# Kernel tuning notes

Measured on AMD Instinct MI355X. Metric: run time of the kernel, lower is better.

Reference implementation:

```python
import jax, jax.numpy as jnp
import numpy as np

GROUPS = 32
EPS = 1e-5


def group_norm(x, gamma, beta):
    B, C, D, H, W = x.shape
    xr = x.reshape(B, GROUPS, C // GROUPS, D, H, W)
    mean = xr.mean(axis=(2, 3, 4, 5), keepdims=True)
    var = xr.var(axis=(2, 3, 4, 5), keepdims=True)
    xn = (xr - mean) * jax.lax.rsqrt(var + EPS)
    xn = xn.reshape(B, C, D, H, W)
    return xn * gamma[None, :, None, None, None] + beta[None, :, None, None, None]


def conv1x1(h, w, b):
    # 1x1x1 Conv3d == channel matmul. w: [O, C], b: [O]
    return jnp.einsum('oc,bcdhw->bodhw', w, h) + b[None, :, None, None, None]


def setup_inputs() -> dict:
    key = jax.random.key(0)
    ks = jax.random.split(key, 10)
    B, C, D, H, W = 2, 128, 16, 16, 16
    x = jax.random.normal(ks[0], (B, C, D, H, W), dtype=jnp.float32)
    gn_w = jnp.ones((C,), dtype=jnp.float32)
    gn_b = jnp.zeros((C,), dtype=jnp.float32)
    # xavier_uniform for [C, C, 1, 1, 1] conv: fan_in = fan_out = C
    lim = float(np.sqrt(6.0 / (C + C)))
    wq = jax.random.uniform(ks[1], (C, C), jnp.float32, -lim, lim)
    wk = jax.random.uniform(ks[2], (C, C), jnp.float32, -lim, lim)
    wv = jax.random.uniform(ks[3], (C, C), jnp.float32, -lim, lim)
    wp = jax.random.uniform(ks[4], (C, C), jnp.float32, -lim, lim) * 1e-05
    bq = jnp.zeros((C,), jnp.float32)
    bk = jnp.zeros((C,), jnp.float32)
    bv = jnp.zeros((C,), jnp.float32)
    bp = jnp.zeros((C,), jnp.float32)
    return {"x": x, "gn_w": gn_w, "gn_b": gn_b, "wq": wq, "bq": bq,
            "wk": wk, "bk": bk, "wv": wv, "bv": bv, "wp": wp, "bp": bp}


def reference(x, gn_w, gn_b, wq, bq, wk, bk, wv, bv, wp, bp):
    B, C, D, H, W = x.shape
    N = D * H * W
    h = group_norm(x, gn_w, gn_b)
    q = conv1x1(h, wq, bq)
    k = conv1x1(h, wk, bk)
    v = conv1x1(h, wv, bv)
    q = q.transpose(0, 2, 3, 4, 1).reshape(B, N, C)   # [B, N, C]
    k = k.reshape(B, C, N)                            # [B, C, N]
    v = v.transpose(0, 2, 3, 4, 1).reshape(B, N, C)   # [B, N, C]
    w = jnp.einsum('bnc,bcm->bnm', q, k) * (C ** -0.5)  # [B, N, N]
    w = jax.nn.softmax(w, axis=-1)
    h = jnp.einsum('bnm,bmc->bnc', w, v)              # [B, N, C]
    h = h.reshape(B, D, H, W, C).transpose(0, 4, 1, 2, 3)
    h = conv1x1(h, wp, bp)
    return x + h
```

## Files before the change

kernel.cpp:

```cpp
#include <hip/hip_runtime.h>
#include <math.h>

#define CC 128
#define NN 4096
#define BB 2
#define NGROUPS 32
#define CPG 4
#define GSIZE (CPG*NN)
#define KSPLIT 2

typedef __attribute__((ext_vector_type(8))) __bf16 bf16x8;
typedef __attribute__((ext_vector_type(4))) float floatx4;

__device__ __forceinline__ unsigned short f2bf(float f) {
  union { float f; unsigned u; } v; v.f = f;
  unsigned r = v.u + 0x7fff + ((v.u >> 16) & 1);
  return (unsigned short)(r >> 16);
}
__device__ __forceinline__ float bf2f(unsigned short u) {
  return __uint_as_float(((unsigned)u) << 16);
}


__global__ void gn_stats_kernel(const float* __restrict__ x, float2* __restrict__ stats) {
  int bid = blockIdx.x;
  int t = threadIdx.x;
  const float4* base = (const float4*)(x + (size_t)bid * 4096);
  float4 v = base[t];
  float s  = v.x + v.y + v.z + v.w;
  float ss = v.x*v.x + v.y*v.y + v.z*v.z + v.w*v.w;
  #pragma unroll
  for (int off = 1; off < 64; off <<= 1) {
    s  += __shfl_xor(s, off);
    ss += __shfl_xor(ss, off);
  }
  __shared__ float sred[4], ssred[4];
  if ((t & 63) == 0) { sred[t >> 6] = s; ssred[t >> 6] = ss; }
  __syncthreads();
  if (t == 0)
    stats[bid] = make_float2(sred[0]+sred[1]+sred[2]+sred[3],
                             ssred[0]+ssred[1]+ssred[2]+ssred[3]);
}

__global__ void prep_kernel(const float2* __restrict__ stats,
                            const float* __restrict__ gamma, const float* __restrict__ beta,
                            const float* __restrict__ wq, const float* __restrict__ bq,
                            const float* __restrict__ wk, const float* __restrict__ wv,
                            const float* __restrict__ wp,
                            float* __restrict__ ab_a, float* __restrict__ ab_b,
                            float* __restrict__ bqs,
                            unsigned short* __restrict__ wqb, unsigned short* __restrict__ wkb,
                            unsigned short* __restrict__ wvb, unsigned short* __restrict__ wpb) {
  const float sc = 0.08838834764831845f;
  int t = threadIdx.x;
  if (blockIdx.x == 64) {
    if (t < BB*NGROUPS) {
      float su = 0.f, ssq = 0.f;
      #pragma unroll
      for (int j = 0; j < 4; j++) { float2 p = stats[t*4 + j]; su += p.x; ssq += p.y; }
      float mean = su * (1.0f/GSIZE);
      float var  = ssq * (1.0f/GSIZE) - mean*mean;
      float rstd = rsqrtf(var + 1e-5f);
      int b = t / NGROUPS, g = t % NGROUPS;
      #pragma unroll
      for (int j = 0; j < 4; j++) {
        int c = g*4 + j;
        float a = rstd * gamma[c];
        ab_a[b*CC + c] = a;
        ab_b[b*CC + c] = beta[c] - mean * a;
      }
    }
    if (t < CC) bqs[t] = bq[t] * sc;
  } else {
    int i = blockIdx.x * 256 + t;
    int id = i >> 12, local = i & 4095;
    const float* src = id==0 ? wq : id==1 ? wk : id==2 ? wv : wp;
    unsigned short* dst = id==0 ? wqb : id==1 ? wkb : id==2 ? wvb : wpb;
    float s = (id == 0) ? sc : 1.0f;
    float4 v = ((const float4*)src)[local];
    unsigned p0 = (unsigned)f2bf(v.x*s) | ((unsigned)f2bf(v.y*s) << 16);
    unsigned p1 = (unsigned)f2bf(v.z*s) | ((unsigned)f2bf(v.w*s) << 16);
    ((uint2*)dst)[local] = make_uint2(p0, p1);
  }
}

__global__ __launch_bounds__(256, 2) void qkv_kernel(
    const float* __restrict__ x,
    const float* __restrict__ ab_a, const float* __restrict__ ab_b,
    const unsigned short* __restrict__ wqb, const unsigned short* __restrict__ wkb,
    const unsigned short* __restrict__ wvb,
    const float* __restrict__ bqs, const float* __restrict__ bk, const float* __restrict__ bv,
    unsigned short* __restrict__ q, unsigned short* __restrict__ k, unsigned short* __restrict__ v) {
  int z = blockIdx.z, b = blockIdx.y, n0 = blockIdx.x * 32;
  const unsigned short* wsel = z==0 ? wqb : z==1 ? wkb : wvb;
  const float* bias          = z==0 ? bqs : z==1 ? bk  : bv;
  unsigned short* outp       = z==0 ? q   : z==1 ? k   : v;
  __shared__ unsigned short hs[32][130];
  __shared__ unsigned short vs[32][136];
  int t = threadIdx.x;
  #pragma unroll
  for (int j = 0; j < 16; j++) {
    int idx = j*256 + t;
    int c = idx >> 5, n = idx & 31;
    float xv = x[((size_t)b*CC + c)*NN + n0 + n];
    hs[n][c] = f2bf(ab_a[b*CC + c]*xv + ab_b[b*CC + c]);
  }
  __syncthreads();
  int w = t >> 6, lane = t & 63, quad = lane >> 4, c = lane & 15;
  int o0 = w * 32;
  floatx4 acc[2][2];
  #pragma unroll
  for (int rt = 0; rt < 2; rt++)
    #pragma unroll
    for (int ct = 0; ct < 2; ct++) acc[rt][ct] = (floatx4){0.f,0.f,0.f,0.f};
  #pragma unroll
  for (int ks = 0; ks < 4; ks++) {
    bf16x8 af[2];
    af[0] = *(const bf16x8*)&hs[c     ][ks*32 + quad*8];
    af[1] = *(const bf16x8*)&hs[16 + c][ks*32 + quad*8];
    #pragma unroll
    for (int ct = 0; ct < 2; ct++) {
      bf16x8 bfr = *(const bf16x8*)(wsel + (size_t)(o0 + ct*16 + c)*CC + ks*32 + quad*8);
      acc[0][ct] = __builtin_amdgcn_mfma_f32_16x16x32_bf16(af[0], bfr, acc[0][ct], 0, 0, 0);
      acc[1][ct] = __builtin_amdgcn_mfma_f32_16x16x32_bf16(af[1], bfr, acc[1][ct], 0, 0, 0);
    }
  }
  if (z < 2) {
    size_t base = (size_t)b*NN*CC + ((size_t)(n0 >> 4))*2048 + w*512;
    #pragma unroll
    for (int ct = 0; ct < 2; ct++) {
      float bi = bias[o0 + ct*16 + c];
      #pragma unroll
      for (int rt = 0; rt < 2; rt++)
        #pragma unroll
        for (int r = 0; r < 4; r++)
          outp[base + rt*2048 + (quad*4 + r)*32 + ct*16 + c] = f2bf(acc[rt][ct][r] + bi);
    }
  } else {
    #pragma unroll
    for (int ct = 0; ct < 2; ct++) {
      float bi = bias[o0 + ct*16 + c];
      #pragma unroll
      for (int rt = 0; rt < 2; rt++)
        #pragma unroll
        for (int r = 0; r < 4; r++)
          vs[rt*16 + quad*4 + r][o0 + ct*16 + c] = f2bf(acc[rt][ct][r] + bi);
    }
    __syncthreads();
    int ct = t >> 5;
    int rem = t & 31;
    int c16 = rem >> 1;
    int m0 = (rem & 1) * 16;
    int ch = ct*16 + c16;
    unsigned pk[8];
    #pragma unroll
    for (int j2 = 0; j2 < 8; j2++) {
      unsigned lo = vs[m0 + j2*2    ][ch];
      unsigned hi = vs[m0 + j2*2 + 1][ch];
      pk[j2] = lo | (hi << 16);
    }
    uint4* dst = (uint4*)(outp + (size_t)b*NN*CC + ((size_t)(n0 >> 5))*4096 + ct*512 + c16*32 + m0);
    dst[0] = make_uint4(pk[0], pk[1], pk[2], pk[3]);
    dst[1] = make_uint4(pk[4], pk[5], pk[6], pk[7]);
  }
}

__global__ __launch_bounds__(256, 2) void attn_kernel(
    const unsigned short* __restrict__ qm,
    const unsigned short* __restrict__ km,
    const unsigned short* __restrict__ vm,
    unsigned short* __restrict__ Opart,
    float* __restrict__ lpart) {
  int b    = blockIdx.z;
  int kh   = blockIdx.y;
  int row0 = blockIdx.x * 32;
  int t    = threadIdx.x;
  int w    = t >> 6, lane = t & 63, quad = lane >> 4, c = lane & 15;

  __shared__ unsigned short shmem[4][32][132];
  __shared__ float lred[4][32];
  unsigned short (*Pl)[72] = (unsigned short (*)[72])&shmem[w][0][0];

  int fragoff = c*32 + quad*8;

  bf16x8 qa[2][4];
  const unsigned short* qbase = qm + (size_t)b*NN*CC + ((size_t)(row0 >> 4))*2048;
  #pragma unroll
  for (int rt = 0; rt < 2; rt++)
    #pragma unroll
    for (int ks = 0; ks < 4; ks++)
      qa[rt][ks] = *(const bf16x8*)(qbase + rt*2048 + ks*512 + fragoff);

  floatx4 O[2][8];
  #pragma unroll
  for (int rt = 0; rt < 2; rt++)
    #pragma unroll
    for (int ct = 0; ct < 8; ct++) O[rt][ct] = (floatx4){0.f,0.f,0.f,0.f};
  float lsum[2][4];
  #pragma unroll
  for (int rt = 0; rt < 2; rt++)
    #pragma unroll
    for (int r = 0; r < 4; r++) lsum[rt][r] = 0.f;

  const unsigned short* kb0 = km + (size_t)b*NN*CC;
  const unsigned short* vb0 = vm + (size_t)b*NN*CC;

  for (int it = 0; it < NN/KSPLIT/256; it++) {
    int mbase = kh*(NN/KSPLIT) + it*256 + w*64;
    const unsigned short* kt = kb0 + ((size_t)(mbase >> 4))*2048;
    const unsigned short* vt = vb0 + ((size_t)(mbase >> 5))*4096;
    floatx4 S[2][4];
    #pragma unroll
    for (int rt = 0; rt < 2; rt++)
      #pragma unroll
      for (int ct = 0; ct < 4; ct++) S[rt][ct] = (floatx4){0.f,0.f,0.f,0.f};
    #pragma unroll
    for (int ks = 0; ks < 4; ks++) {
      #pragma unroll
      for (int ct = 0; ct < 4; ct++) {
        bf16x8 kf = *(const bf16x8*)(kt + ct*2048 + ks*512 + fragoff);
        S[0][ct] = __builtin_amdgcn_mfma_f32_16x16x32_bf16(qa[0][ks], kf, S[0][ct], 0, 0, 0);
        S[1][ct] = __builtin_amdgcn_mfma_f32_16x16x32_bf16(qa[1][ks], kf, S[1][ct], 0, 0, 0);
      }
    }
    #pragma unroll
    for (int rt = 0; rt < 2; rt++) {
      #pragma unroll
      for (int ct = 0; ct < 4; ct++) {
        float e0 = __expf(S[rt][ct][0]);
        float e1 = __expf(S[rt][ct][1]);
        float e2 = __expf(S[rt][ct][2]);
        float e3 = __expf(S[rt][ct][3]);
        lsum[rt][0] += e0; lsum[rt][1] += e1;
        lsum[rt][2] += e2; lsum[rt][3] += e3;
        bool odd = (c & 1);
        float s01 = odd ? e0 : e1;
        float g01 = __shfl_xor(s01, 1);
        unsigned lo0 = __float_as_uint(odd ? g01 : e0);
        unsigned hi0 = __float_as_uint(odd ? e1 : g01);
        unsigned p0 = (hi0 & 0xffff0000u) | (lo0 >> 16);
        float s23 = odd ? e2 : e3;
        float g23 = __shfl_xor(s23, 1);
        unsigned lo1 = __float_as_uint(odd ? g23 : e2);
        unsigned hi1 = __float_as_uint(odd ? e3 : g23);
        unsigned p1 = (hi1 & 0xffff0000u) | (lo1 >> 16);
        int colpair = ct*16 + (c & ~1);
        int rowA = rt*16 + quad*4 + (odd ? 1 : 0);
        int rowB = rt*16 + quad*4 + (odd ? 3 : 2);
        *(unsigned*)&Pl[rowA][colpair] = p0;
        *(unsigned*)&Pl[rowB][colpair] = p1;
      }
    }
    #pragma unroll
    for (int ks2 = 0; ks2 < 2; ks2++) {
      bf16x8 pa0 = *(const bf16x8*)(&Pl[c     ][ks2*32 + quad*8]);
      bf16x8 pa1 = *(const bf16x8*)(&Pl[16 + c][ks2*32 + quad*8]);
      #pragma unroll
      for (int ct = 0; ct < 8; ct++) {
        bf16x8 vf = *(const bf16x8*)(vt + ks2*4096 + ct*512 + fragoff);
        O[0][ct] = __builtin_amdgcn_mfma_f32_16x16x32_bf16(pa0, vf, O[0][ct], 0, 0, 0);
        O[1][ct] = __builtin_amdgcn_mfma_f32_16x16x32_bf16(pa1, vf, O[1][ct], 0, 0, 0);
      }
    }
  }

  #pragma unroll
  for (int rt = 0; rt < 2; rt++)
    #pragma unroll
    for (int r = 0; r < 4; r++) {
      float vsum = lsum[rt][r];
      vsum += __shfl_xor(vsum, 1);
      vsum += __shfl_xor(vsum, 2);
      vsum += __shfl_xor(vsum, 4);
      vsum += __shfl_xor(vsum, 8);
      if (c == 0) lred[w][rt*16 + quad*4 + r] = vsum;
    }
  __syncthreads();
  #pragma unroll
  for (int rt = 0; rt < 2; rt++)
    #pragma unroll
    for (int ct = 0; ct < 8; ct++)
      #pragma unroll
      for (int r = 0; r < 4; r++)
        shmem[w][rt*16 + quad*4 + r][ct*16 + c] = f2bf(O[rt][ct][r]);
  __syncthreads();
  size_t pbase = (size_t)(kh*BB + b)*NN + row0;
  if (t < 32)
    lpart[pbase + t] = lred[0][t] + lred[1][t] + lred[2][t] + lred[3][t];
  int rr = t >> 3, c0 = (t & 7) * 16;
  unsigned pk[8];
  #pragma unroll
  for (int j2 = 0; j2 < 8; j2++) {
    int cc0 = c0 + j2*2;
    float v0 = bf2f(shmem[0][rr][cc0])   + bf2f(shmem[1][rr][cc0])
             + bf2f(shmem[2][rr][cc0])   + bf2f(shmem[3][rr][cc0]);
    float v1 = bf2f(shmem[0][rr][cc0+1]) + bf2f(shmem[1][rr][cc0+1])
             + bf2f(shmem[2][rr][cc0+1]) + bf2f(shmem[3][rr][cc0+1]);
    pk[j2] = (unsigned)f2bf(v0) | ((unsigned)f2bf(v1) << 16);
  }
  uint4* od = (uint4*)(Opart + (pbase + rr)*CC + c0);
  od[0] = make_uint4(pk[0], pk[1], pk[2], pk[3]);
  od[1] = make_uint4(pk[4], pk[5], pk[6], pk[7]);
}

__global__ __launch_bounds__(256, 2) void combine_kernel(
    const unsigned short* __restrict__ Opart, const float* __restrict__ lpart,
    const unsigned short* __restrict__ wpb, const float* __restrict__ bp,
    const float* __restrict__ x, float* __restrict__ out) {
  int b = blockIdx.y, n0 = blockIdx.x * 32;
  int t = threadIdx.x;
  __shared__ unsigned short hs[32][130];
  __shared__ float ps[32][132];
  __shared__ float linv[32];
  if (t < 32) {
    float l = 0.f;
    #pragma unroll
    for (int kh = 0; kh < KSPLIT; kh++)
      l += lpart[((size_t)(kh*BB + b))*NN + n0 + t];
    linv[t] = 1.f / l;
  }
  __syncthreads();
  #pragma unroll
  for (int j = 0; j < 16; j++) {
    int idx = j*256 + t;
    int n = idx >> 7, c2 = idx & 127;
    float o = 0.f;
    #pragma unroll
    for (int kh = 0; kh < KSPLIT; kh++)
      o += bf2f(Opart[((size_t)(kh*BB + b)*NN + n0 + n)*CC + c2]);
    hs[n][c2] = f2bf(o * linv[n]);
  }
  __syncthreads();
  int w = t >> 6, lane = t & 63, quad = lane >> 4, c = lane & 15;
  int o0 = w * 32;
  floatx4 acc[2][2];
  #pragma unroll
  for (int rt = 0; rt < 2; rt++)
    #pragma unroll
    for (int ct = 0; ct < 2; ct++) acc[rt][ct] = (floatx4){0.f,0.f,0.f,0.f};
  #pragma unroll
  for (int ks = 0; ks < 4; ks++) {
    bf16x8 af[2];
    af[0] = *(const bf16x8*)&hs[c     ][ks*32 + quad*8];
    af[1] = *(const bf16x8*)&hs[16 + c][ks*32 + quad*8];
    #pragma unroll
    for (int ct = 0; ct < 2; ct++) {
      bf16x8 bfr = *(const bf16x8*)(wpb + (size_t)(o0 + ct*16 + c)*CC + ks*32 + quad*8);
      acc[0][ct] = __builtin_amdgcn_mfma_f32_16x16x32_bf16(af[0], bfr, acc[0][ct], 0, 0, 0);
      acc[1][ct] = __builtin_amdgcn_mfma_f32_16x16x32_bf16(af[1], bfr, acc[1][ct], 0, 0, 0);
    }
  }
  #pragma unroll
  for (int rt = 0; rt < 2; rt++)
    #pragma unroll
    for (int ct = 0; ct < 2; ct++)
      #pragma unroll
      for (int r = 0; r < 4; r++)
        ps[rt*16 + quad*4 + r][o0 + ct*16 + c] = acc[rt][ct][r];
  __syncthreads();
  int o = t >> 1, nh = (t & 1) * 16;
  float bi = bp[o];
  const float* xr = x + ((size_t)b*CC + o)*NN + n0 + nh;
  float* orow = out + ((size_t)b*CC + o)*NN + n0 + nh;
  #pragma unroll
  for (int j4 = 0; j4 < 4; j4++) {
    float4 xv = ((const float4*)xr)[j4];
    float4 ov;
    ov.x = xv.x + ps[nh + j4*4 + 0][o] + bi;
    ov.y = xv.y + ps[nh + j4*4 + 1][o] + bi;
    ov.z = xv.z + ps[nh + j4*4 + 2][o] + bi;
    ov.w = xv.w + ps[nh + j4*4 + 3][o] + bi;
    ((float4*)orow)[j4] = ov;
  }
}

extern "C" void kernel_launch(void* const* d_in, const int* in_sizes, int n_in,
                              void* d_out, int out_size, void* d_ws, size_t ws_size,
                              hipStream_t stream) {
  const float* x    = (const float*)d_in[0];
  const float* gn_w = (const float*)d_in[1];
  const float* gn_b = (const float*)d_in[2];
  const float* wq   = (const float*)d_in[3];
  const float* bq   = (const float*)d_in[4];
  const float* wk   = (const float*)d_in[5];
  const float* bk   = (const float*)d_in[6];
  const float* wv   = (const float*)d_in[7];
  const float* bv   = (const float*)d_in[8];
  const float* wp   = (const float*)d_in[9];
  const float* bp   = (const float*)d_in[10];
  float* out = (float*)d_out;

  char* ws = (char*)d_ws;
  float2*         stats = (float2*)(ws);
  float*          ab_a  = (float*)(ws + 2048);
  float*          ab_b  = (float*)(ws + 3072);
  float*          bqs   = (float*)(ws + 4096);
  unsigned short* wqb   = (unsigned short*)(ws + 8192);
  unsigned short* wkb   = (unsigned short*)(ws + 8192 + 32768);
  unsigned short* wvb   = (unsigned short*)(ws + 8192 + 65536);
  unsigned short* wpb   = (unsigned short*)(ws + 8192 + 98304);
  unsigned short* qb    = (unsigned short*)(ws + 262144);
  unsigned short* kb    = (unsigned short*)(ws + 262144 + 2097152);
  unsigned short* vb    = (unsigned short*)(ws + 262144 + 2*2097152);
  unsigned short* Opart = (unsigned short*)(ws + 262144 + 3*2097152);
  float*          lpart = (float*)(ws + 262144 + 3*2097152 + 4194304);

  gn_stats_kernel<<<dim3(256), 256, 0, stream>>>(x, stats);
  prep_kernel    <<<dim3(65), 256, 0, stream>>>(stats, gn_w, gn_b, wq, bq, wk, wv, wp,
                                                ab_a, ab_b, bqs, wqb, wkb, wvb, wpb);
  qkv_kernel     <<<dim3(NN/32, BB, 3), 256, 0, stream>>>(x, ab_a, ab_b, wqb, wkb, wvb,
                                                          bqs, bk, bv, qb, kb, vb);
  attn_kernel    <<<dim3(NN/32, KSPLIT, BB), 256, 0, stream>>>(qb, kb, vb, Opart, lpart);
  combine_kernel <<<dim3(NN/32, BB), 256, 0, stream>>>(Opart, lpart, wpb, bp, x, out);
}
```

Measured before the change: 134.6 us.

## Merge prep into stats kernel, fold GN finalize into qkv, prefetch K fragments

The weight bf16 conversion now runs in extra blocks of the stats kernel, and the group-norm mean/rstd finalisation moves into each qkv block, computed in shared memory. This removes one kernel launch and the small prep dependency stage, at the cost of redundant per-block stats work. In the attention loop, the K fragments for the next iteration are loaded into registers while softmax and PV run, to hide global load latency. This adds register pressure from the 16-entry kfn array.

```diff
diff --git a/kernel.cpp b/kernel.cpp
--- a/kernel.cpp
+++ b/kernel.cpp
@@ -22,57 +22,32 @@
 }
 
 
-__global__ void gn_stats_kernel(const float* __restrict__ x, float2* __restrict__ stats) {
-  int bid = blockIdx.x;
+__global__ void gn_stats_kernel(const float* __restrict__ x, float2* __restrict__ stats,
+                                const float* __restrict__ wq, const float* __restrict__ wk,
+                                const float* __restrict__ wv, const float* __restrict__ wp,
+                                unsigned short* __restrict__ wqb, unsigned short* __restrict__ wkb,
+                                unsigned short* __restrict__ wvb, unsigned short* __restrict__ wpb) {
   int t = threadIdx.x;
-  const float4* base = (const float4*)(x + (size_t)bid * 4096);
-  float4 v = base[t];
-  float s  = v.x + v.y + v.z + v.w;
-  float ss = v.x*v.x + v.y*v.y + v.z*v.z + v.w*v.w;
-  #pragma unroll
-  for (int off = 1; off < 64; off <<= 1) {
-    s  += __shfl_xor(s, off);
-    ss += __shfl_xor(ss, off);
-  }
-  __shared__ float sred[4], ssred[4];
-  if ((t & 63) == 0) { sred[t >> 6] = s; ssred[t >> 6] = ss; }
-  __syncthreads();
-  if (t == 0)
-    stats[bid] = make_float2(sred[0]+sred[1]+sred[2]+sred[3],
-                             ssred[0]+ssred[1]+ssred[2]+ssred[3]);
-}
-
-__global__ void prep_kernel(const float2* __restrict__ stats,
-                            const float* __restrict__ gamma, const float* __restrict__ beta,
-                            const float* __restrict__ wq, const float* __restrict__ bq,
-                            const float* __restrict__ wk, const float* __restrict__ wv,
-                            const float* __restrict__ wp,
-                            float* __restrict__ ab_a, float* __restrict__ ab_b,
-                            float* __restrict__ bqs,
-                            unsigned short* __restrict__ wqb, unsigned short* __restrict__ wkb,
-                            unsigned short* __restrict__ wvb, unsigned short* __restrict__ wpb) {
-  const float sc = 0.08838834764831845f;
-  int t = threadIdx.x;
-  if (blockIdx.x == 64) {
-    if (t < BB*NGROUPS) {
-      float su = 0.f, ssq = 0.f;
-      #pragma unroll
-      for (int j = 0; j < 4; j++) { float2 p = stats[t*4 + j]; su += p.x; ssq += p.y; }
-      float mean = su * (1.0f/GSIZE);
-      float var  = ssq * (1.0f/GSIZE) - mean*mean;
-      float rstd = rsqrtf(var + 1e-5f);
-      int b = t / NGROUPS, g = t % NGROUPS;
-      #pragma unroll
-      for (int j = 0; j < 4; j++) {
-        int c = g*4 + j;
-        float a = rstd * gamma[c];
-        ab_a[b*CC + c] = a;
-        ab_b[b*CC + c] = beta[c] - mean * a;
-      }
-    }
-    if (t < CC) bqs[t] = bq[t] * sc;
+  if (blockIdx.x < 256) {
+    int bid = blockIdx.x;
+    const float4* base = (const float4*)(x + (size_t)bid * 4096);
+    float4 v = base[t];
+    float s  = v.x + v.y + v.z + v.w;
+    float ss = v.x*v.x + v.y*v.y + v.z*v.z + v.w*v.w;
+    #pragma unroll
+    for (int off = 1; off < 64; off <<= 1) {
+      s  += __shfl_xor(s, off);
+      ss += __shfl_xor(ss, off);
+    }
+    __shared__ float sred[4], ssred[4];
+    if ((t & 63) == 0) { sred[t >> 6] = s; ssred[t >> 6] = ss; }
+    __syncthreads();
+    if (t == 0)
+      stats[bid] = make_float2(sred[0]+sred[1]+sred[2]+sred[3],
+                               ssred[0]+ssred[1]+ssred[2]+ssred[3]);
   } else {
-    int i = blockIdx.x * 256 + t;
+    const float sc = 0.08838834764831845f;
+    int i = (blockIdx.x - 256) * 256 + t;
     int id = i >> 12, local = i & 4095;
     const float* src = id==0 ? wq : id==1 ? wk : id==2 ? wv : wp;
     unsigned short* dst = id==0 ? wqb : id==1 ? wkb : id==2 ? wvb : wpb;
@@ -85,25 +60,47 @@
 }
 
 __global__ __launch_bounds__(256, 2) void qkv_kernel(
-    const float* __restrict__ x,
-    const float* __restrict__ ab_a, const float* __restrict__ ab_b,
+    const float* __restrict__ x, const float2* __restrict__ stats,
+    const float* __restrict__ gamma, const float* __restrict__ beta,
     const unsigned short* __restrict__ wqb, const unsigned short* __restrict__ wkb,
     const unsigned short* __restrict__ wvb,
-    const float* __restrict__ bqs, const float* __restrict__ bk, const float* __restrict__ bv,
+    const float* __restrict__ bq, const float* __restrict__ bk, const float* __restrict__ bv,
     unsigned short* __restrict__ q, unsigned short* __restrict__ k, unsigned short* __restrict__ v) {
   int z = blockIdx.z, b = blockIdx.y, n0 = blockIdx.x * 32;
   const unsigned short* wsel = z==0 ? wqb : z==1 ? wkb : wvb;
-  const float* bias          = z==0 ? bqs : z==1 ? bk  : bv;
+  const float* bias          = z==0 ? bq  : z==1 ? bk  : bv;
+  float bscale               = z==0 ? 0.08838834764831845f : 1.0f;
   unsigned short* outp       = z==0 ? q   : z==1 ? k   : v;
   __shared__ unsigned short hs[32][130];
   __shared__ unsigned short vs[32][136];
+  __shared__ float gm[NGROUPS], gr[NGROUPS], aa[CC], ab[CC];
   int t = threadIdx.x;
+  if (t < NGROUPS) {
+    float su = 0.f, ssq = 0.f;
+    #pragma unroll
+    for (int j = 0; j < 4; j++) {
+      float2 p = stats[(b*NGROUPS + t)*4 + j];
+      su += p.x; ssq += p.y;
+    }
+    float mean = su * (1.0f/GSIZE);
+    float var  = ssq * (1.0f/GSIZE) - mean*mean;
+    gm[t] = mean;
+    gr[t] = rsqrtf(var + 1e-5f);
+  }
+  __syncthreads();
+  if (t < CC) {
+    int g = t >> 2;
+    float a = gr[g] * gamma[t];
+    aa[t] = a;
+    ab[t] = beta[t] - gm[g] * a;
+  }
+  __syncthreads();
   #pragma unroll
   for (int j = 0; j < 16; j++) {
     int idx = j*256 + t;
     int c = idx >> 5, n = idx & 31;
     float xv = x[((size_t)b*CC + c)*NN + n0 + n];
-    hs[n][c] = f2bf(ab_a[b*CC + c]*xv + ab_b[b*CC + c]);
+    hs[n][c] = f2bf(aa[c]*xv + ab[c]);
   }
   __syncthreads();
   int w = t >> 6, lane = t & 63, quad = lane >> 4, c = lane & 15;
@@ -129,7 +126,7 @@
     size_t base = (size_t)b*NN*CC + ((size_t)(n0 >> 4))*2048 + w*512;
     #pragma unroll
     for (int ct = 0; ct < 2; ct++) {
-      float bi = bias[o0 + ct*16 + c];
+      float bi = bias[o0 + ct*16 + c] * bscale;
       #pragma unroll
       for (int rt = 0; rt < 2; rt++)
         #pragma unroll
@@ -204,11 +201,21 @@
 
   const unsigned short* kb0 = km + (size_t)b*NN*CC;
   const unsigned short* vb0 = vm + (size_t)b*NN*CC;
-
-  for (int it = 0; it < NN/KSPLIT/256; it++) {
-    int mbase = kh*(NN/KSPLIT) + it*256 + w*64;
-    const unsigned short* kt = kb0 + ((size_t)(mbase >> 4))*2048;
-    const unsigned short* vt = vb0 + ((size_t)(mbase >> 5))*4096;
+  const unsigned short* ktbase = kb0 + ((size_t)(kh*128 + w*4))*2048;
+  const unsigned short* vtbase = vb0 + ((size_t)(kh*64  + w*2))*4096;
+
+  const int ITERS = NN/KSPLIT/256;
+
+  bf16x8 kf[4][4];
+  #pragma unroll
+  for (int ks = 0; ks < 4; ks++)
+    #pragma unroll
+    for (int ct = 0; ct < 4; ct++)
+      kf[ks][ct] = *(const bf16x8*)(ktbase + ct*2048 + ks*512 + fragoff);
+
+  for (int it = 0; it < ITERS; it++) {
+    const unsigned short* vt  = vtbase + (size_t)it*32768;
+    const unsigned short* ktn = ktbase + (size_t)((it+1 < ITERS) ? it+1 : it)*32768;
     floatx4 S[2][4];
     #pragma unroll
     for (int rt = 0; rt < 2; rt++)
@@ -218,11 +225,16 @@
     for (int ks = 0; ks < 4; ks++) {
       #pragma unroll
       for (int ct = 0; ct < 4; ct++) {
-        bf16x8 kf = *(const bf16x8*)(kt + ct*2048 + ks*512 + fragoff);
-        S[0][ct] = __builtin_amdgcn_mfma_f32_16x16x32_bf16(qa[0][ks], kf, S[0][ct], 0, 0, 0);
-        S[1][ct] = __builtin_amdgcn_mfma_f32_16x16x32_bf16(qa[1][ks], kf, S[1][ct], 0, 0, 0);
+        S[0][ct] = __builtin_amdgcn_mfma_f32_16x16x32_bf16(qa[0][ks], kf[ks][ct], S[0][ct], 0, 0, 0);
+        S[1][ct] = __builtin_amdgcn_mfma_f32_16x16x32_bf16(qa[1][ks], kf[ks][ct], S[1][ct], 0, 0, 0);
       }
     }
+    bf16x8 kfn[4][4];
+    #pragma unroll
+    for (int ks = 0; ks < 4; ks++)
+      #pragma unroll
+      for (int ct = 0; ct < 4; ct++)
+        kfn[ks][ct] = *(const bf16x8*)(ktn + ct*2048 + ks*512 + fragoff);
     #pragma unroll
     for (int rt = 0; rt < 2; rt++) {
       #pragma unroll
@@ -262,6 +274,11 @@
         O[1][ct] = __builtin_amdgcn_mfma_f32_16x16x32_bf16(pa1, vf, O[1][ct], 0, 0, 0);
       }
     }
+    #pragma unroll
+    for (int ks = 0; ks < 4; ks++)
+      #pragma unroll
+      for (int ct = 0; ct < 4; ct++)
+        kf[ks][ct] = kfn[ks][ct];
   }
 
   #pragma unroll
@@ -392,9 +409,6 @@
 
   char* ws = (char*)d_ws;
   float2*         stats = (float2*)(ws);
-  float*          ab_a  = (float*)(ws + 2048);
-  float*          ab_b  = (float*)(ws + 3072);
-  float*          bqs   = (float*)(ws + 4096);
   unsigned short* wqb   = (unsigned short*)(ws + 8192);
   unsigned short* wkb   = (unsigned short*)(ws + 8192 + 32768);
   unsigned short* wvb   = (unsigned short*)(ws + 8192 + 65536);
@@ -405,11 +419,11 @@
   unsigned short* Opart = (unsigned short*)(ws + 262144 + 3*2097152);
   float*          lpart = (float*)(ws + 262144 + 3*2097152 + 4194304);
 
-  gn_stats_kernel<<<dim3(256), 256, 0, stream>>>(x, stats);
-  prep_kernel    <<<dim3(65), 256, 0, stream>>>(stats, gn_w, gn_b, wq, bq, wk, wv, wp,
-                                                ab_a, ab_b, bqs, wqb, wkb, wvb, wpb);
-  qkv_kernel     <<<dim3(NN/32, BB, 3), 256, 0, stream>>>(x, ab_a, ab_b, wqb, wkb, wvb,
-                                                          bqs, bk, bv, qb, kb, vb);
+  gn_stats_kernel<<<dim3(320), 256, 0, stream>>>(x, stats, wq, wk, wv, wp,
+                                                 wqb, wkb, wvb, wpb);
+  qkv_kernel     <<<dim3(NN/32, BB, 3), 256, 0, stream>>>(x, stats, gn_w, gn_b,
+                                                          wqb, wkb, wvb, bq, bk, bv,
+                                                          qb, kb, vb);
   attn_kernel    <<<dim3(NN/32, KSPLIT, BB), 256, 0, stream>>>(qb, kb, vb, Opart, lpart);
   combine_kernel <<<dim3(NN/32, BB), 256, 0, stream>>>(Opart, lpart, wpb, bp, x, out);
 }
```

New measurement: 124.4 us. 1.08x faster.
